# Kernel tuning notes

Hardware: AMD Instinct MI355X
Metric: run time of the kernel (lower is better)

Reference implementation:

```python
import jax, jax.numpy as jnp
import numpy as np

B = 262144
MA = [128, 128]
MB = [128, 128]


def krone_linear(x_a, x_b, wa, wb, ba, bb):
    # slice inputs to each branch's in_features (torch slices the wider branch)
    ia, ib = wa.shape[1], wb.shape[1]
    x_a = x_a[:, :ia]
    x_b = x_b[:, :ib]
    h_a = x_a @ wa.T + ba
    h_b = x_b @ wb.T + bb
    # zero-pad the narrower output so both branches share a width (static shapes)
    oa, ob = wa.shape[0], wb.shape[0]
    if oa > ob:
        h_b = jnp.pad(h_b, ((0, 0), (0, oa - ob)))
    elif ob > oa:
        h_a = jnp.pad(h_a, ((0, 0), (0, ob - oa)))
    return h_a, h_b


def krone_softmax(x_a, x_b, fa, fb):
    x_a = x_a[:, :fa]
    x_b = x_b[:, :fb]
    # vectorized per-row Kronecker product: kron(a, b)[i*fb + j] = a[i]*b[j]
    y = (x_a[:, :, None] * x_b[:, None, :]).reshape(x_a.shape[0], fa * fb)
    return jax.nn.softmax(y, axis=1)


def setup_inputs() -> dict:
    key = jax.random.key(0)
    ks = jax.random.split(key, 13)
    s = 0.1
    inp = {
        "x": jax.random.normal(ks[0], (2, B, 2), dtype=jnp.float32),
        "w1a": jax.random.normal(ks[1], (MA[0], 2), dtype=jnp.float32) * s,
        "w1b": jax.random.normal(ks[2], (MB[0], 2), dtype=jnp.float32) * s,
        "b1a": jax.random.normal(ks[3], (MA[0],), dtype=jnp.float32) * s,
        "b1b": jax.random.normal(ks[4], (MB[0],), dtype=jnp.float32) * s,
        "w2a": jax.random.normal(ks[5], (MA[1], MA[0]), dtype=jnp.float32) * s,
        "w2b": jax.random.normal(ks[6], (MB[1], MB[0]), dtype=jnp.float32) * s,
        "b2a": jax.random.normal(ks[7], (MA[1],), dtype=jnp.float32) * s,
        "b2b": jax.random.normal(ks[8], (MB[1],), dtype=jnp.float32) * s,
        "w3a": jax.random.normal(ks[9], (1, MA[1]), dtype=jnp.float32) * s,
        "w3b": jax.random.normal(ks[10], (3, MB[1]), dtype=jnp.float32) * s,
        "b3a": jax.random.normal(ks[11], (1,), dtype=jnp.float32) * s,
        "b3b": jax.random.normal(ks[12], (3,), dtype=jnp.float32) * s,
    }
    return inp


def reference(x, w1a, w1b, b1a, b1b, w2a, w2b, b2a, b2b, w3a, w3b, b3a, b3b):
    x_a, x_b = x[0], x[1]
    h_a, h_b = krone_linear(x_a, x_b, w1a, w1b, b1a, b1b)
    h_a, h_b = jax.nn.relu(h_a), jax.nn.relu(h_b)
    h_a, h_b = krone_linear(h_a, h_b, w2a, w2b, b2a, b2b)
    h_a, h_b = jax.nn.relu(h_a), jax.nn.relu(h_b)
    h_a, h_b = krone_linear(h_a, h_b, w3a, w3b, b3a, b3b)
    return krone_softmax(h_a, h_b, 1, 3)
```

## Files before the change

kernel.cpp:

```cpp
#include <hip/hip_runtime.h>
#include <hip/hip_bf16.h>


#define BTOT 262144
#define NBLK (BTOT / 512)

typedef __attribute__((ext_vector_type(4))) float floatx4;
typedef __attribute__((ext_vector_type(8))) short bf16x8;
typedef __attribute__((ext_vector_type(4))) int  intx4;

#define OFF_W2  0
#define OFF_W1  32768
#define OFF_B2  35072
#define OFF_W3  35584
#define OFF_SA  37120
#define LDS_TOTAL 39168

static __device__ __forceinline__ int pack2bf(float lo, float hi) {
    unsigned a = __builtin_bit_cast(unsigned, lo) + 0x8000u;
    unsigned b = __builtin_bit_cast(unsigned, hi) + 0x8000u;
    return (int)__builtin_amdgcn_perm(b, a, 0x07060302u);
}

#define SEL4(a0, a1, a2, a3, i) \
    ((i) == 0 ? (a0) : (i) == 1 ? (a1) : (i) == 2 ? (a2) : (a3))

static __device__ __forceinline__ float redcol(float v) {
    v += __shfl_xor(v, 1); v += __shfl_xor(v, 2);
    v += __shfl_xor(v, 4); v += __shfl_xor(v, 8);
    return v;
}

static __device__ __forceinline__ int w1slot(int k) { return k + (k >> 3); }

static __device__ __forceinline__ void pack_path(
        unsigned char* smem, int tid,
        const float* __restrict__ w2, const float* __restrict__ w1,
        const float* __restrict__ b1, const float* __restrict__ b2) {
    const float4* w2p = (const float4*)w2;
    #pragma unroll
    for (int i = 0; i < 8; ++i) {
        int n  = (tid & 15) | (i << 4);
        int k4 = tid >> 4;
        float4 f = w2p[n * 32 + k4];
        int k = k4 * 4;
        int s = k >> 5;
        int j0 = k & 7;
        int l = ((k & 31) >> 3) * 16 + (n & 15);
        int2 pkd;
        pkd.x = pack2bf(f.x, f.y);
        pkd.y = pack2bf(f.z, f.w);
        *(int2*)(smem + OFF_W2 + (s * 8 + (n >> 4)) * 1024 + l * 16 + j0 * 2) = pkd;
    }
    if (tid < 128) {
        ((float4*)(smem + OFF_W1))[w1slot(tid)] =
            make_float4(w1[2 * tid], w1[2 * tid + 1], b1[tid], 0.f);
        ((float*)(smem + OFF_B2))[tid] = b2[tid];
    }
}

#define GEMM_CHUNK(acc, XV, W1p, W2p, B2p)                                     \
    {                                                                          \
        _Pragma("unroll")                                                      \
        for (int t = 0; t < 8; ++t) {                                          \
            float b2n = (B2p)[t * 16 + col];                                   \
            floatx4 bi = (floatx4){b2n, b2n, b2n, b2n};                        \
            _Pragma("unroll")                                                  \
            for (int mt = 0; mt < 2; ++mt) acc[t][mt] = bi;                    \
        }                                                                      \
        _Pragma("unroll")                                                      \
        for (int s = 0; s < 4; ++s) {                                          \
            intx4 af[2];                                                       \
            const int bslot = s * 36 + quad * 9;                               \
            _Pragma("unroll")                                                  \
            for (int j2 = 0; j2 < 4; ++j2) {                                   \
                float4 c0 = (W1p)[bslot + 2 * j2];                             \
                float4 c1 = (W1p)[bslot + 2 * j2 + 1];                         \
                _Pragma("unroll")                                              \
                for (int mt = 0; mt < 2; ++mt) {                               \
                    float h0 = fmaxf(fmaf((XV)[mt].x, c0.x,                    \
                                fmaf((XV)[mt].y, c0.y, c0.z)), 0.f);           \
                    float h1 = fmaxf(fmaf((XV)[mt].x, c1.x,                    \
                                fmaf((XV)[mt].y, c1.y, c1.z)), 0.f);           \
                    af[mt][j2] = pack2bf(h0, h1);                              \
                }                                                              \
            }                                                                  \
            _Pragma("unroll")                                                  \
            for (int t = 0; t < 8; ++t) {                                      \
                bf16x8 bfr = (W2p)[(s * 8 + t) * 64 + lane];                   \
                _Pragma("unroll")                                              \
                for (int mt = 0; mt < 2; ++mt)                                 \
                    acc[t][mt] = __builtin_amdgcn_mfma_f32_16x16x32_bf16(      \
                        __builtin_bit_cast(bf16x8, af[mt]), bfr,               \
                        acc[t][mt], 0, 0, 0);                                  \
            }                                                                  \
        }                                                                      \
    }

__global__ __launch_bounds__(512, 4)
void krone_fused(const float* __restrict__ x,
                 const float* __restrict__ w1a, const float* __restrict__ w1b,
                 const float* __restrict__ b1a, const float* __restrict__ b1b,
                 const float* __restrict__ w2a, const float* __restrict__ w2b,
                 const float* __restrict__ b2a, const float* __restrict__ b2b,
                 const float* __restrict__ w3a, const float* __restrict__ w3b,
                 const float* __restrict__ b3a, const float* __restrict__ b3b,
                 float* __restrict__ out) {
    __shared__ __align__(16) unsigned char smem[LDS_TOTAL];

    const int tid  = threadIdx.x;
    const int lane = tid & 63;
    const int wave = tid >> 6;
    const int quad = lane >> 4;
    const int col  = lane & 15;
    const int wbase = blockIdx.x * 512 + wave * 64;

    const bf16x8* W2 = (const bf16x8*)(smem + OFF_W2);
    const float4* W1 = (const float4*)(smem + OFF_W1);
    const float*  B2 = (const float*)(smem + OFF_B2);
    const float*  W3 = (const float*)(smem + OFF_W3);
    float*        SA = (float*)(smem + OFF_SA);
    const float2* xA = (const float2*)x;
    const float2* xB = xA + BTOT;

    const float b3a_ = b3a[0];
    const float b30 = b3b[0], b31 = b3b[1], b32 = b3b[2];

    float2 xv[4];
    #pragma unroll
    for (int c = 0; c < 2; ++c)
        #pragma unroll
        for (int mt = 0; mt < 2; ++mt)
            xv[c * 2 + mt] = xA[wbase + c * 32 + mt * 16 + col];

    pack_path(smem, tid, w2a, w1a, b1a, b2a);
    if (tid < 128) ((float*)(smem + OFF_W3))[tid] = w3a[tid];
    __syncthreads();

    #pragma unroll
    for (int c = 0; c < 2; ++c) {
        __builtin_amdgcn_sched_barrier(0);
        floatx4 acc[8][2];
        GEMM_CHUNK(acc, xv + 2 * c, W1, W2, B2);
        __builtin_amdgcn_sched_barrier(0);

        float pa[2][4] = {};
        #pragma unroll
        for (int t = 0; t < 8; ++t) {
            float w3n = W3[t * 16 + col];
            #pragma unroll
            for (int mt = 0; mt < 2; ++mt)
                #pragma unroll
                for (int r = 0; r < 4; ++r)
                    pa[mt][r] = fmaf(w3n, fmaxf(acc[t][mt][r], 0.f), pa[mt][r]);
        }
        #pragma unroll
        for (int mt = 0; mt < 2; ++mt)
            #pragma unroll
            for (int r = 0; r < 4; ++r) pa[mt][r] = redcol(pa[mt][r]);
        __builtin_amdgcn_sched_barrier(0);

        if (col < 4) {
            #pragma unroll
            for (int mt = 0; mt < 2; ++mt) {
                int sl = mt * 16 + quad * 4 + col;
                SA[wave * 64 + c * 32 + sl] =
                    SEL4(pa[mt][0], pa[mt][1], pa[mt][2], pa[mt][3], col) + b3a_;
            }
        }
        __builtin_amdgcn_sched_barrier(0);
    }

    #pragma unroll
    for (int c = 0; c < 2; ++c)
        #pragma unroll
        for (int mt = 0; mt < 2; ++mt)
            xv[c * 2 + mt] = xB[wbase + c * 32 + mt * 16 + col];

    __syncthreads();
    pack_path(smem, tid, w2b, w1b, b1b, b2b);
    if (tid < 384) ((float*)(smem + OFF_W3))[tid] = w3b[tid];
    __syncthreads();

    #pragma unroll
    for (int c = 0; c < 2; ++c) {
        __builtin_amdgcn_sched_barrier(0);
        floatx4 acc[8][2];
        GEMM_CHUNK(acc, xv + 2 * c, W1, W2, B2);
        __builtin_amdgcn_sched_barrier(0);

        #pragma unroll
        for (int mt = 0; mt < 2; ++mt) {
            float p0[4] = {}, p1[4] = {}, p2[4] = {};
            #pragma unroll
            for (int t = 0; t < 8; ++t) {
                int n = t * 16 + col;
                float w30 = W3[n], w31 = W3[128 + n], w32 = W3[256 + n];
                #pragma unroll
                for (int r = 0; r < 4; ++r) {
                    float h = fmaxf(acc[t][mt][r], 0.f);
                    p0[r] = fmaf(w30, h, p0[r]);
                    p1[r] = fmaf(w31, h, p1[r]);
                    p2[r] = fmaf(w32, h, p2[r]);
                }
            }
            #pragma unroll
            for (int r = 0; r < 4; ++r) {
                p0[r] = redcol(p0[r]);
                p1[r] = redcol(p1[r]);
                p2[r] = redcol(p2[r]);
            }
            if (col < 4) {
                int sl = mt * 16 + quad * 4 + col;
                float t0 = SEL4(p0[0], p0[1], p0[2], p0[3], col) + b30;
                float t1 = SEL4(p1[0], p1[1], p1[2], p1[3], col) + b31;
                float t2 = SEL4(p2[0], p2[1], p2[2], p2[3], col) + b32;
                float sa = SA[wave * 64 + c * 32 + sl];
                float y0 = sa * t0, y1 = sa * t1, y2 = sa * t2;
                float m = fmaxf(y0, fmaxf(y1, y2));
                float e0 = __expf(y0 - m), e1 = __expf(y1 - m), e2 = __expf(y2 - m);
                float rs = 1.f / (e0 + e1 + e2);
                long o = (long)(wbase + c * 32 + sl) * 3;
                out[o]     = e0 * rs;
                out[o + 1] = e1 * rs;
                out[o + 2] = e2 * rs;
            }
        }
        __builtin_amdgcn_sched_barrier(0);
    }
}

extern "C" void kernel_launch(void* const* d_in, const int* in_sizes, int n_in,
                              void* d_out, int out_size, void* d_ws, size_t ws_size,
                              hipStream_t stream) {
    const float* x   = (const float*)d_in[0];
    const float* w1a = (const float*)d_in[1];
    const float* w1b = (const float*)d_in[2];
    const float* b1a = (const float*)d_in[3];
    const float* b1b = (const float*)d_in[4];
    const float* w2a = (const float*)d_in[5];
    const float* w2b = (const float*)d_in[6];
    const float* b2a = (const float*)d_in[7];
    const float* b2b = (const float*)d_in[8];
    const float* w3a = (const float*)d_in[9];
    const float* w3b = (const float*)d_in[10];
    const float* b3a = (const float*)d_in[11];
    const float* b3b = (const float*)d_in[12];
    float* out = (float*)d_out;

    krone_fused<<<NBLK, 512, 0, stream>>>(x, w1a, w1b, b1a, b1b, w2a, w2b,
                                          b2a, b2b, w3a, w3b, b3a, b3b, out);
}
```

Measured before the change: 109.9 us.

## Prestage B-path small weights, use DPP reductions and hardware bf16 packing

Stages both paths' W1/B1/B2 and W3 at kernel start so the mid-kernel restage only repacks W2. W3b is stored transposed so one float4 LDS read replaces three scalar reads. The column reduction now uses DPP row operations instead of ds_swizzle/shfl, and packing uses v_cvt_pk_bf16_f32. LDS use grows slightly, which could affect occupancy, and the hardware convert rounds differently from the old round-half-up bias.

```diff
diff --git a/kernel.cpp b/kernel.cpp
--- a/kernel.cpp
+++ b/kernel.cpp
@@ -9,34 +9,43 @@
 typedef __attribute__((ext_vector_type(8))) short bf16x8;
 typedef __attribute__((ext_vector_type(4))) int  intx4;
 
-#define OFF_W2  0
-#define OFF_W1  32768
-#define OFF_B2  35072
-#define OFF_W3  35584
-#define OFF_SA  37120
-#define LDS_TOTAL 39168
+#define OFF_W2   0
+#define OFF_W1A  32768
+#define OFF_W1B  35072
+#define OFF_B2A  37376
+#define OFF_B2B  37888
+#define OFF_W3A  38400
+#define OFF_W3B  38912
+#define OFF_SA   40960
+#define LDS_TOTAL 43008
 
 static __device__ __forceinline__ int pack2bf(float lo, float hi) {
-    unsigned a = __builtin_bit_cast(unsigned, lo) + 0x8000u;
-    unsigned b = __builtin_bit_cast(unsigned, hi) + 0x8000u;
-    return (int)__builtin_amdgcn_perm(b, a, 0x07060302u);
+    int r;
+    asm("v_cvt_pk_bf16_f32 %0, %1, %2" : "=v"(r) : "v"(lo), "v"(hi));
+    return r;
 }
 
 #define SEL4(a0, a1, a2, a3, i) \
     ((i) == 0 ? (a0) : (i) == 1 ? (a1) : (i) == 2 ? (a2) : (a3))
 
+template <int CTRL>
+static __device__ __forceinline__ float dppadd(float v) {
+    int t = __builtin_amdgcn_update_dpp(0, __builtin_bit_cast(int, v),
+                                        CTRL, 0xF, 0xF, true);
+    return v + __builtin_bit_cast(float, t);
+}
 static __device__ __forceinline__ float redcol(float v) {
-    v += __shfl_xor(v, 1); v += __shfl_xor(v, 2);
-    v += __shfl_xor(v, 4); v += __shfl_xor(v, 8);
+    v = dppadd<0xB1>(v);
+    v = dppadd<0x4E>(v);
+    v = dppadd<0x141>(v);
+    v = dppadd<0x140>(v);
     return v;
 }
 
 static __device__ __forceinline__ int w1slot(int k) { return k + (k >> 3); }
 
-static __device__ __forceinline__ void pack_path(
-        unsigned char* smem, int tid,
-        const float* __restrict__ w2, const float* __restrict__ w1,
-        const float* __restrict__ b1, const float* __restrict__ b2) {
+static __device__ __forceinline__ void pack_w2(
+        unsigned char* smem, int tid, const float* __restrict__ w2) {
     const float4* w2p = (const float4*)w2;
     #pragma unroll
     for (int i = 0; i < 8; ++i) {
@@ -52,10 +61,16 @@
         pkd.y = pack2bf(f.z, f.w);
         *(int2*)(smem + OFF_W2 + (s * 8 + (n >> 4)) * 1024 + l * 16 + j0 * 2) = pkd;
     }
+}
+
+static __device__ __forceinline__ void stage_small(
+        unsigned char* smem, int tid, int offW1, int offB2,
+        const float* __restrict__ w1, const float* __restrict__ b1,
+        const float* __restrict__ b2) {
     if (tid < 128) {
-        ((float4*)(smem + OFF_W1))[w1slot(tid)] =
+        ((float4*)(smem + offW1))[w1slot(tid)] =
             make_float4(w1[2 * tid], w1[2 * tid + 1], b1[tid], 0.f);
-        ((float*)(smem + OFF_B2))[tid] = b2[tid];
+        ((float*)(smem + offB2))[tid] = b2[tid];
     }
 }
 
@@ -115,11 +130,14 @@
     const int col  = lane & 15;
     const int wbase = blockIdx.x * 512 + wave * 64;
 
-    const bf16x8* W2 = (const bf16x8*)(smem + OFF_W2);
-    const float4* W1 = (const float4*)(smem + OFF_W1);
-    const float*  B2 = (const float*)(smem + OFF_B2);
-    const float*  W3 = (const float*)(smem + OFF_W3);
-    float*        SA = (float*)(smem + OFF_SA);
+    const bf16x8* W2  = (const bf16x8*)(smem + OFF_W2);
+    const float4* W1A = (const float4*)(smem + OFF_W1A);
+    const float4* W1B = (const float4*)(smem + OFF_W1B);
+    const float*  B2A = (const float*)(smem + OFF_B2A);
+    const float*  B2B = (const float*)(smem + OFF_B2B);
+    const float*  W3A = (const float*)(smem + OFF_W3A);
+    const float4* W3T = (const float4*)(smem + OFF_W3B);
+    float*        SA  = (float*)(smem + OFF_SA);
     const float2* xA = (const float2*)x;
     const float2* xB = xA + BTOT;
 
@@ -133,21 +151,27 @@
         for (int mt = 0; mt < 2; ++mt)
             xv[c * 2 + mt] = xA[wbase + c * 32 + mt * 16 + col];
 
-    pack_path(smem, tid, w2a, w1a, b1a, b2a);
-    if (tid < 128) ((float*)(smem + OFF_W3))[tid] = w3a[tid];
+    pack_w2(smem, tid, w2a);
+    stage_small(smem, tid, OFF_W1A, OFF_B2A, w1a, b1a, b2a);
+    stage_small(smem, tid, OFF_W1B, OFF_B2B, w1b, b1b, b2b);
+    if (tid < 128) ((float*)(smem + OFF_W3A))[tid] = w3a[tid];
+    if (tid < 384) {
+        int j = tid >> 7, n = tid & 127;
+        ((float*)(smem + OFF_W3B))[n * 4 + j] = w3b[tid];
+    }
     __syncthreads();
 
     #pragma unroll
     for (int c = 0; c < 2; ++c) {
         __builtin_amdgcn_sched_barrier(0);
         floatx4 acc[8][2];
-        GEMM_CHUNK(acc, xv + 2 * c, W1, W2, B2);
+        GEMM_CHUNK(acc, xv + 2 * c, W1A, W2, B2A);
         __builtin_amdgcn_sched_barrier(0);
 
         float pa[2][4] = {};
         #pragma unroll
         for (int t = 0; t < 8; ++t) {
-            float w3n = W3[t * 16 + col];
+            float w3n = W3A[t * 16 + col];
             #pragma unroll
             for (int mt = 0; mt < 2; ++mt)
                 #pragma unroll
@@ -178,15 +202,14 @@
             xv[c * 2 + mt] = xB[wbase + c * 32 + mt * 16 + col];
 
     __syncthreads();
-    pack_path(smem, tid, w2b, w1b, b1b, b2b);
-    if (tid < 384) ((float*)(smem + OFF_W3))[tid] = w3b[tid];
+    pack_w2(smem, tid, w2b);
     __syncthreads();
 
     #pragma unroll
     for (int c = 0; c < 2; ++c) {
         __builtin_amdgcn_sched_barrier(0);
         floatx4 acc[8][2];
-        GEMM_CHUNK(acc, xv + 2 * c, W1, W2, B2);
+        GEMM_CHUNK(acc, xv + 2 * c, W1B, W2, B2B);
         __builtin_amdgcn_sched_barrier(0);
 
         #pragma unroll
@@ -194,14 +217,13 @@
             float p0[4] = {}, p1[4] = {}, p2[4] = {};
             #pragma unroll
             for (int t = 0; t < 8; ++t) {
-                int n = t * 16 + col;
-                float w30 = W3[n], w31 = W3[128 + n], w32 = W3[256 + n];
+                float4 w3v = W3T[t * 16 + col];
                 #pragma unroll
                 for (int r = 0; r < 4; ++r) {
                     float h = fmaxf(acc[t][mt][r], 0.f);
-                    p0[r] = fmaf(w30, h, p0[r]);
-                    p1[r] = fmaf(w31, h, p1[r]);
-                    p2[r] = fmaf(w32, h, p2[r]);
+                    p0[r] = fmaf(w3v.x, h, p0[r]);
+                    p1[r] = fmaf(w3v.y, h, p1[r]);
+                    p2[r] = fmaf(w3v.z, h, p2[r]);
                 }
             }
             #pragma unroll
```

After: 105.7 us. -3.8%, faster.
